# Kernel optimization log

Measured on AMD Instinct MI355X. Metric: run time of the kernel, lower is better.

Reference implementation:

```python
import jax, jax.numpy as jnp
import numpy as np

B, A, F = 8192, 8, 256      # batch, n_agents, per-agent obs feature dim
NA = 16                     # n_actions per agent
H1, H2 = 1024, 1024
OBS_D = A * F               # 2048 flattened obs dim
ACT_D = A * NA              # 128 joint action dim
IN_D = OBS_D + ACT_D        # 2176 MLP input dim


def setup_inputs() -> dict:
    key = jax.random.key(0)
    ks = jax.random.split(key, 8)
    s = 0.02
    return {
        "obs": jax.random.normal(ks[0], (B, A, F), dtype=jnp.float32),
        "all_actions": jax.random.uniform(ks[1], (B, ACT_D), dtype=jnp.float32),
        # per-agent stacked MLP params (agent axis first)
        "W1": jax.random.normal(ks[2], (A, IN_D, H1), dtype=jnp.float32) * s,
        "b1": jnp.zeros((A, H1), dtype=jnp.float32),
        "W2": jax.random.normal(ks[3], (A, H1, H2), dtype=jnp.float32) * s,
        "b2": jnp.zeros((A, H2), dtype=jnp.float32),
        "W3": jax.random.normal(ks[4], (A, H2, NA), dtype=jnp.float32) * s,
        "b3": jnp.zeros((A, NA), dtype=jnp.float32),
    }


def reference(obs, all_actions, W1, b1, W2, b2, W3, b3):
    b_s = obs.shape[0]
    obs_flat = obs.reshape(b_s, OBS_D)                      # [B, A*F]
    # mask[a, g] = 0 on agent a's own action block, 1 elsewhere
    mask = 1.0 - jnp.repeat(jnp.eye(A, dtype=obs.dtype), NA, axis=1)  # [A, A*NA]
    # split W1 into obs / action columns (equivalent to concat-then-dense)
    W1o = W1[:, :OBS_D, :]                                  # [A, OBS_D, H1]
    W1a = W1[:, OBS_D:, :]                                  # [A, ACT_D, H1]
    h1 = jax.nn.relu(
        jnp.einsum("bd,adh->bah", obs_flat, W1o)
        + jnp.einsum("bg,ag,agh->bah", all_actions, mask, W1a)
        + b1
    )                                                        # [B, A, H1]
    h2 = jax.nn.relu(jnp.einsum("bah,ahk->bak", h1, W2) + b2)  # [B, A, H2]
    out = jnp.einsum("bak,akn->ban", h2, W3) + b3              # [B, A, NA]
    return out.reshape(b_s, A * NA)
```

## Files before the change

kernel.cpp:

```cpp
#include <hip/hip_runtime.h>
#include <hip/hip_bf16.h>
#include <cstdint>
#include <cstddef>

typedef __bf16 bf16;
typedef __attribute__((ext_vector_type(8))) __bf16 bf16x8;
typedef __attribute__((ext_vector_type(4))) float f32x4;
typedef __attribute__((ext_vector_type(4))) int i32x4;
typedef __attribute__((address_space(3))) const bf16* lds_cp;

#define B_SZ  8192
#define NAGENT 8
#define NA_N  16
#define OBS_DD 2048
#define ACT_DD 128
#define IN_DD 2176
#define H1_D  1024
#define H2_D  1024

#define BM 256
#define BN 256
#define BK 64
#define GRID_M (B_SZ / BM)
#define GRID_N (1024 / BN)

__device__ __forceinline__ void gload16(const void* g, void* l) {
    __builtin_amdgcn_global_load_lds(
        (__attribute__((address_space(1))) void*)(g),
        (__attribute__((address_space(3))) void*)(l), 16, 0, 0);
}


__global__ void k_convert_x(const float* __restrict__ obs,
                            const float* __restrict__ act,
                            bf16* __restrict__ xb) {
    const int chunks = IN_DD / 8;
    int idx = blockIdx.x * blockDim.x + threadIdx.x;
    if (idx >= B_SZ * chunks) return;
    int b = idx / chunks;
    int c8 = idx - b * chunks;
    const float* src = (c8 < OBS_DD / 8)
        ? (obs + (size_t)b * OBS_DD + c8 * 8)
        : (act + (size_t)b * ACT_DD + (c8 - OBS_DD / 8) * 8);
    float4 v0 = ((const float4*)src)[0];
    float4 v1 = ((const float4*)src)[1];
    bf16x8 o;
    o[0] = (bf16)v0.x; o[1] = (bf16)v0.y; o[2] = (bf16)v0.z; o[3] = (bf16)v0.w;
    o[4] = (bf16)v1.x; o[5] = (bf16)v1.y; o[6] = (bf16)v1.z; o[7] = (bf16)v1.w;
    ((bf16x8*)(xb + (size_t)b * IN_DD))[c8] = o;
}

__global__ void k_transpose_w(const float* __restrict__ src, bf16* __restrict__ dst,
                              int K, int H, int maskStart) {
    __shared__ float tile[32][33];
    int a = blockIdx.z;
    int k0 = blockIdx.x * 32, h0 = blockIdx.y * 32;
    const float* s = src + (size_t)a * K * H;
    bf16* d = dst + (size_t)a * K * H;
    int tx = threadIdx.x, ty = threadIdx.y;
    #pragma unroll
    for (int i = 0; i < 32; i += 8) {
        int k = k0 + ty + i;
        float v = s[(size_t)k * H + h0 + tx];
        if (k >= maskStart) {
            int g = k - maskStart;
            if ((g >> 4) == a) v = 0.f;
        }
        tile[ty + i][tx] = v;
    }
    __syncthreads();
    #pragma unroll
    for (int i = 0; i < 32; i += 8) {
        d[(size_t)(h0 + ty + i) * K + k0 + tx] = (bf16)tile[tx][ty + i];
    }
}

__global__ void k_transpose_w3(const float* __restrict__ src, bf16* __restrict__ dst) {
    int idx = blockIdx.x * blockDim.x + threadIdx.x;
    if (idx >= NAGENT * NA_N * H2_D) return;
    int a = idx / (NA_N * H2_D);
    int n = (idx / H2_D) % NA_N;
    int k = idx % H2_D;
    dst[idx] = (bf16)src[(size_t)a * H2_D * NA_N + (size_t)k * NA_N + n];
}

__global__ void k_init_out(const float* __restrict__ b3, float* __restrict__ out) {
    int i = blockIdx.x * blockDim.x + threadIdx.x;
    if (i < B_SZ * NAGENT * NA_N) out[i] = b3[i & 127];
}

#define DSR4(d0, d1, d2, d3, addr, O0, O1, O2, O3)                      \
    asm volatile("ds_read_b128 %0, %4 offset:" #O0 "\n\t"               \
                 "ds_read_b128 %1, %4 offset:" #O1 "\n\t"               \
                 "ds_read_b128 %2, %4 offset:" #O2 "\n\t"               \
                 "ds_read_b128 %3, %4 offset:" #O3                      \
                 : "=&v"(d0), "=&v"(d1), "=&v"(d2), "=&v"(d3)           \
                 : "v"(addr))

#define BC(x) __builtin_bit_cast(bf16x8, x)

template<int FUSE>
__global__ __launch_bounds__(512, 2)
void k_gemm256(const bf16* __restrict__ Ain, size_t aStride, int lda,
               const bf16* __restrict__ Bw, const float* __restrict__ bias,
               bf16* __restrict__ Cout, size_t cStride, int K,
               int aOff, int gridZ,
               const bf16* __restrict__ W3Tp, float* __restrict__ outp) {
    extern __shared__ bf16 lds[];

    const int tid = threadIdx.x;
    const int w = tid >> 6;
    const int l = tid & 63;

    int flat = blockIdx.x + GRID_M * (blockIdx.y + GRID_N * blockIdx.z);
    int q8 = (GRID_M * GRID_N * gridZ) >> 3;
    int lin2 = (flat & 7) * q8 + (flat >> 3);
    const int mt = lin2 % GRID_M;
    int rest = lin2 / GRID_M;
    const int ntile = rest % GRID_N;
    const int az = rest / GRID_N;
    const int aw = az + aOff;

    const int rowBase = mt * BM;
    const int colBase = ntile * BN;
    const bf16* Aag = Ain + (size_t)az * aStride;
    const bf16* Bag = Bw + (size_t)aw * (size_t)1024 * K;

    const int wr = (w >> 2) * 128;
    const int wc = (w & 3) * 64;
    const int lr = l & 15;
    const int lq = l >> 4;

    const int rowA = (wr + lr) * BK;
    const int rowB = (wc + lr) * BK;
    const int ck0 = ((lq ^ (lr & 7)) * 8);
    const int ck1 = (((4 + lq) ^ (lr & 7)) * 8);

    const int sRow = w * 16 + (l >> 3);
    const int sCol = ((l & 7) ^ (l >> 3)) * 8;

    const bf16* pA0 = Aag + (size_t)(rowBase + sRow) * lda + sCol;
    const bf16* pA1 = Aag + (size_t)(rowBase + 128 + sRow) * lda + sCol;
    const bf16* pB0 = Bag + (size_t)(colBase + sRow) * K + sCol;
    const bf16* pB1 = Bag + (size_t)(colBase + 128 + sRow) * K + sCol;
    const size_t l8a = (size_t)8 * lda;
    const size_t l8b = (size_t)8 * K;

    const int nkt = K / BK;

#define STAGE_A(t1, half) do {                                              \
        const bf16* g_ = ((half) ? pA1 : pA0) + (t1) * BK;                  \
        bf16* d_ = &lds[(((t1) & 1) * 32768) + (half) * 8192 + w * 1024];   \
        gload16(g_, d_);                                                    \
        gload16(g_ + l8a, d_ + 512);                                        \
    } while (0)
#define STAGE_B(t2, half) do {                                              \
        const bf16* g_ = ((half) ? pB1 : pB0) + (t2) * BK;                  \
        bf16* d_ = &lds[(((t2) & 1) * 32768) + 16384 + (half) * 8192 + w * 1024]; \
        gload16(g_, d_);                                                    \
        gload16(g_ + l8b, d_ + 512);                                        \
    } while (0)

    f32x4 acc[8][4] = {};
    i32x4 ra0, ra1, ra2, ra3;
    i32x4 rb0, rb1, rb2, rb3;
    i32x4 rc0, rc1, rc2, rc3;

    STAGE_A(0, 0); STAGE_A(0, 1);
    STAGE_B(0, 0); STAGE_B(0, 1);
    if (nkt > 1) { STAGE_B(1, 0); STAGE_B(1, 1); }
    asm volatile("s_waitcnt vmcnt(0)" ::: "memory");
    __builtin_amdgcn_s_barrier();

    for (int t = 0; t < nkt; ++t) {
        const int dbuf = (t & 1) * 32768;
        lds_cp adrA0 = (lds_cp)lds + (dbuf + rowA + ck0);
        lds_cp adrA1 = (lds_cp)lds + (dbuf + rowA + ck1);
        lds_cp adrB0 = (lds_cp)lds + (dbuf + 16384 + rowB + ck0);
        lds_cp adrB1 = (lds_cp)lds + (dbuf + 16384 + rowB + ck1);

        DSR4(ra0, ra1, ra2, ra3, adrA0, 0, 2048, 4096, 6144);
        DSR4(rb0, rb1, rb2, rb3, adrB0, 0, 2048, 4096, 6144);
        if (t + 1 < nkt) STAGE_A(t + 1, 0);
        __builtin_amdgcn_s_barrier();
        asm volatile("s_waitcnt lgkmcnt(0)" ::: "memory");
        __builtin_amdgcn_sched_barrier(0);
        __builtin_amdgcn_s_setprio(1);
        #pragma unroll
        for (int n = 0; n < 4; ++n) {
            bf16x8 bv = BC(n == 0 ? rb0 : n == 1 ? rb1 : n == 2 ? rb2 : rb3);
            acc[0][n] = __builtin_amdgcn_mfma_f32_16x16x32_bf16(BC(ra0), bv, acc[0][n], 0, 0, 0);
            acc[1][n] = __builtin_amdgcn_mfma_f32_16x16x32_bf16(BC(ra1), bv, acc[1][n], 0, 0, 0);
            acc[2][n] = __builtin_amdgcn_mfma_f32_16x16x32_bf16(BC(ra2), bv, acc[2][n], 0, 0, 0);
            acc[3][n] = __builtin_amdgcn_mfma_f32_16x16x32_bf16(BC(ra3), bv, acc[3][n], 0, 0, 0);
        }
        __builtin_amdgcn_s_setprio(0);
        __builtin_amdgcn_s_barrier();

        DSR4(ra0, ra1, ra2, ra3, adrA0, 8192, 10240, 12288, 14336);
        DSR4(rc0, rc1, rc2, rc3, adrB1, 0, 2048, 4096, 6144);
        if (t + 1 < nkt) STAGE_A(t + 1, 1);
        __builtin_amdgcn_s_barrier();
        asm volatile("s_waitcnt lgkmcnt(0)" ::: "memory");
        __builtin_amdgcn_sched_barrier(0);
        __builtin_amdgcn_s_setprio(1);
        #pragma unroll
        for (int n = 0; n < 4; ++n) {
            bf16x8 bv = BC(n == 0 ? rb0 : n == 1 ? rb1 : n == 2 ? rb2 : rb3);
            acc[4][n] = __builtin_amdgcn_mfma_f32_16x16x32_bf16(BC(ra0), bv, acc[4][n], 0, 0, 0);
            acc[5][n] = __builtin_amdgcn_mfma_f32_16x16x32_bf16(BC(ra1), bv, acc[5][n], 0, 0, 0);
            acc[6][n] = __builtin_amdgcn_mfma_f32_16x16x32_bf16(BC(ra2), bv, acc[6][n], 0, 0, 0);
            acc[7][n] = __builtin_amdgcn_mfma_f32_16x16x32_bf16(BC(ra3), bv, acc[7][n], 0, 0, 0);
        }
        __builtin_amdgcn_s_setprio(0);
        __builtin_amdgcn_s_barrier();

        DSR4(ra0, ra1, ra2, ra3, adrA1, 0, 2048, 4096, 6144);
        if (t + 2 < nkt) STAGE_B(t + 2, 0);
        __builtin_amdgcn_s_barrier();
        asm volatile("s_waitcnt lgkmcnt(0)" ::: "memory");
        __builtin_amdgcn_sched_barrier(0);
        __builtin_amdgcn_s_setprio(1);
        #pragma unroll
        for (int n = 0; n < 4; ++n) {
            bf16x8 bv = BC(n == 0 ? rc0 : n == 1 ? rc1 : n == 2 ? rc2 : rc3);
            acc[0][n] = __builtin_amdgcn_mfma_f32_16x16x32_bf16(BC(ra0), bv, acc[0][n], 0, 0, 0);
            acc[1][n] = __builtin_amdgcn_mfma_f32_16x16x32_bf16(BC(ra1), bv, acc[1][n], 0, 0, 0);
            acc[2][n] = __builtin_amdgcn_mfma_f32_16x16x32_bf16(BC(ra2), bv, acc[2][n], 0, 0, 0);
            acc[3][n] = __builtin_amdgcn_mfma_f32_16x16x32_bf16(BC(ra3), bv, acc[3][n], 0, 0, 0);
        }
        __builtin_amdgcn_s_setprio(0);
        __builtin_amdgcn_s_barrier();

        DSR4(ra0, ra1, ra2, ra3, adrA1, 8192, 10240, 12288, 14336);
        if (t + 2 < nkt) STAGE_B(t + 2, 1);
        __builtin_amdgcn_s_barrier();
        asm volatile("s_waitcnt lgkmcnt(0)" ::: "memory");
        __builtin_amdgcn_sched_barrier(0);
        __builtin_amdgcn_s_setprio(1);
        #pragma unroll
        for (int n = 0; n < 4; ++n) {
            bf16x8 bv = BC(n == 0 ? rc0 : n == 1 ? rc1 : n == 2 ? rc2 : rc3);
            acc[4][n] = __builtin_amdgcn_mfma_f32_16x16x32_bf16(BC(ra0), bv, acc[4][n], 0, 0, 0);
            acc[5][n] = __builtin_amdgcn_mfma_f32_16x16x32_bf16(BC(ra1), bv, acc[5][n], 0, 0, 0);
            acc[6][n] = __builtin_amdgcn_mfma_f32_16x16x32_bf16(BC(ra2), bv, acc[6][n], 0, 0, 0);
            acc[7][n] = __builtin_amdgcn_mfma_f32_16x16x32_bf16(BC(ra3), bv, acc[7][n], 0, 0, 0);
        }
        __builtin_amdgcn_s_setprio(0);
        if (t < nkt - 2) {
            asm volatile("s_waitcnt vmcnt(4)" ::: "memory");
        } else {
            asm volatile("s_waitcnt vmcnt(0)" ::: "memory");
        }
        __builtin_amdgcn_s_barrier();
    }
#undef STAGE_A
#undef STAGE_B

    __syncthreads();
    const float* bAg = bias + (size_t)aw * 1024;
    float bb4[4];
    #pragma unroll
    for (int n = 0; n < 4; ++n) bb4[n] = bAg[colBase + wc + n * 16 + lr];
    #pragma unroll
    for (int m = 0; m < 8; ++m)
        #pragma unroll
        for (int n = 0; n < 4; ++n)
            #pragma unroll
            for (int r = 0; r < 4; ++r) {
                float v = acc[m][n][r] + bb4[n];
                v = fmaxf(v, 0.f);
                int row = wr + m * 16 + lq * 4 + r;
                int col = wc + n * 16 + lr;
                lds[row * 256 + ((((col >> 3) ^ (row & 7)) << 3) | (col & 7))] = (bf16)v;
            }
    __syncthreads();

    if constexpr (!FUSE) {
        bf16* Cg = Cout + (size_t)az * cStride + (size_t)rowBase * 1024 + colBase;
        const int er = tid >> 5;
        const int ec = tid & 31;
        #pragma unroll
        for (int i = 0; i < 16; ++i) {
            int row = i * 16 + er;
            int phys = ec ^ (row & 7);
            *(bf16x8*)&Cg[(size_t)row * 1024 + ec * 8] =
                *(const bf16x8*)&lds[row * 256 + phys * 8];
        }
    } else {
        const bf16* w3a = W3Tp + (size_t)aw * NA_N * H2_D;
        f32x4 oacc[2] = {};
        const int frow0 = w * 32;
        #pragma unroll
        for (int ks = 0; ks < 8; ++ks) {
            bf16x8 bfrag = *(const bf16x8*)&w3a[(size_t)lr * H2_D + colBase + ks * 32 + lq * 8];
            #pragma unroll
            for (int mm = 0; mm < 2; ++mm) {
                int row = frow0 + mm * 16 + lr;
                int lc = (ks * 4 + lq) ^ (row & 7);
                bf16x8 afrag = *(const bf16x8*)&lds[row * 256 + lc * 8];
                oacc[mm] = __builtin_amdgcn_mfma_f32_16x16x32_bf16(afrag, bfrag, oacc[mm], 0, 0, 0);
            }
        }
        #pragma unroll
        for (int mm = 0; mm < 2; ++mm)
            #pragma unroll
            for (int r = 0; r < 4; ++r)
                atomicAdd(&outp[(size_t)(rowBase + frow0 + mm * 16 + lq * 4 + r) * 128
                                + aw * NA_N + lr], oacc[mm][r]);
    }
}

extern "C" void kernel_launch(void* const* d_in, const int* in_sizes, int n_in,
                              void* d_out, int out_size, void* d_ws, size_t ws_size,
                              hipStream_t stream) {
    const float* obs = (const float*)d_in[0];
    const float* act = (const float*)d_in[1];
    const float* W1 = (const float*)d_in[2];
    const float* b1 = (const float*)d_in[3];
    const float* W2 = (const float*)d_in[4];
    const float* b2 = (const float*)d_in[5];
    const float* W3 = (const float*)d_in[6];
    const float* b3 = (const float*)d_in[7];
    float* out = (float*)d_out;

    const size_t SZ_XB  = (size_t)B_SZ * IN_DD * 2;
    const size_t SZ_W1T = (size_t)NAGENT * H1_D * IN_DD * 2;
    const size_t SZ_W2T = (size_t)NAGENT * H1_D * H2_D * 2;
    const size_t SZ_W3T = (size_t)NAGENT * NA_N * H2_D * 2;
    const size_t SZ_H1  = (size_t)B_SZ * H1_D * 2;
    const size_t SZ_FIX = SZ_XB + SZ_W1T + SZ_W2T + SZ_W3T;

    char* ws = (char*)d_ws;
    bf16* Xb  = (bf16*)ws;
    bf16* W1T = (bf16*)(ws + SZ_XB);
    bf16* W2T = (bf16*)(ws + SZ_XB + SZ_W1T);
    bf16* W3T = (bf16*)(ws + SZ_XB + SZ_W1T + SZ_W2T);
    char* hbase = ws + SZ_FIX;

    int G = 8;
    while (G > 1 && ws_size < SZ_FIX + (size_t)G * SZ_H1) G >>= 1;

    (void)hipFuncSetAttribute((const void*)k_gemm256<0>,
                              hipFuncAttributeMaxDynamicSharedMemorySize, 131072);
    (void)hipFuncSetAttribute((const void*)k_gemm256<1>,
                              hipFuncAttributeMaxDynamicSharedMemorySize, 131072);

    k_init_out<<<(B_SZ * 128 + 255) / 256, 256, 0, stream>>>(b3, out);

    {
        int n = B_SZ * (IN_DD / 8);
        k_convert_x<<<(n + 255) / 256, 256, 0, stream>>>(obs, act, Xb);
    }
    k_transpose_w<<<dim3(IN_DD / 32, H1_D / 32, NAGENT), dim3(32, 8), 0, stream>>>(
        W1, W1T, IN_DD, H1_D, OBS_DD);
    k_transpose_w<<<dim3(H1_D / 32, H2_D / 32, NAGENT), dim3(32, 8), 0, stream>>>(
        W2, W2T, H1_D, H2_D, 1 << 30);
    {
        int n = NAGENT * NA_N * H2_D;
        k_transpose_w3<<<(n + 255) / 256, 256, 0, stream>>>(W3, W3T);
    }

    const size_t agElems = (size_t)B_SZ * H1_D;
    bf16* h1 = (bf16*)hbase;

    for (int g0 = 0; g0 < NAGENT; g0 += G) {
        k_gemm256<0><<<dim3(GRID_M, GRID_N, G), 512, 131072, stream>>>(
            Xb, 0, IN_DD, W1T, b1, h1, agElems, IN_DD, g0, G, nullptr, nullptr);
        k_gemm256<1><<<dim3(GRID_M, GRID_N, G), 512, 131072, stream>>>(
            h1, agElems, H1_D, W2T, b2, nullptr, 0, H1_D, g0, G, W3T, out);
    }
    (void)in_sizes; (void)n_in; (void)out_size;
}
```

Baseline: 472.1 us.

## Switch GEMM mainloop to BK=32 with four-stage LDS ring pipeline

Halves the K-tile to 32 and replaces the two-buffer LDS scheme with a four-slot ring that prefetches three tiles ahead, staging A and B for tile t+3 while computing tile t. Hand-written ds_read_b128 inline asm and explicit lgkmcnt waits are replaced by plain vector LDS loads, leaving scheduling to the compiler. The intent is deeper latency hiding of global loads and fewer barriers per MFMA. In exchange each iteration does less MFMA work relative to its barriers, the swizzle narrows to 4 chunks, and the compiler may place LDS waits less carefully than the manual asm did.

```diff
diff --git a/kernel.cpp b/kernel.cpp
--- a/kernel.cpp
+++ b/kernel.cpp
@@ -6,8 +6,6 @@
 typedef __bf16 bf16;
 typedef __attribute__((ext_vector_type(8))) __bf16 bf16x8;
 typedef __attribute__((ext_vector_type(4))) float f32x4;
-typedef __attribute__((ext_vector_type(4))) int i32x4;
-typedef __attribute__((address_space(3))) const bf16* lds_cp;
 
 #define B_SZ  8192
 #define NAGENT 8
@@ -20,7 +18,7 @@
 
 #define BM 256
 #define BN 256
-#define BK 64
+#define BK 32
 #define GRID_M (B_SZ / BM)
 #define GRID_N (1024 / BN)
 
@@ -89,16 +87,6 @@
     if (i < B_SZ * NAGENT * NA_N) out[i] = b3[i & 127];
 }
 
-#define DSR4(d0, d1, d2, d3, addr, O0, O1, O2, O3)                      \
-    asm volatile("ds_read_b128 %0, %4 offset:" #O0 "\n\t"               \
-                 "ds_read_b128 %1, %4 offset:" #O1 "\n\t"               \
-                 "ds_read_b128 %2, %4 offset:" #O2 "\n\t"               \
-                 "ds_read_b128 %3, %4 offset:" #O3                      \
-                 : "=&v"(d0), "=&v"(d1), "=&v"(d2), "=&v"(d3)           \
-                 : "v"(addr))
-
-#define BC(x) __builtin_bit_cast(bf16x8, x)
-
 template<int FUSE>
 __global__ __launch_bounds__(512, 2)
 void k_gemm256(const bf16* __restrict__ Ain, size_t aStride, int lda,
@@ -131,123 +119,81 @@
     const int lr = l & 15;
     const int lq = l >> 4;
 
-    const int rowA = (wr + lr) * BK;
-    const int rowB = (wc + lr) * BK;
-    const int ck0 = ((lq ^ (lr & 7)) * 8);
-    const int ck1 = (((4 + lq) ^ (lr & 7)) * 8);
-
-    const int sRow = w * 16 + (l >> 3);
-    const int sCol = ((l & 7) ^ (l >> 3)) * 8;
-
-    const bf16* pA0 = Aag + (size_t)(rowBase + sRow) * lda + sCol;
-    const bf16* pA1 = Aag + (size_t)(rowBase + 128 + sRow) * lda + sCol;
-    const bf16* pB0 = Bag + (size_t)(colBase + sRow) * K + sCol;
-    const bf16* pB1 = Bag + (size_t)(colBase + 128 + sRow) * K + sCol;
-    const size_t l8a = (size_t)8 * lda;
-    const size_t l8b = (size_t)8 * K;
+    const int swz = (lq ^ (lr & 3)) * 8;
+    const int rA = (wr + lr) * 32 + swz;
+    const int rB = 8192 + (wc + lr) * 32 + swz;
+
+    const int sR = w * 16 + (l >> 2);
+    const int sC = ((l & 3) ^ ((l >> 2) & 3)) * 8;
+    const bf16* pA0 = Aag + (size_t)(rowBase + sR) * lda + sC;
+    const bf16* pA1 = Aag + (size_t)(rowBase + 128 + sR) * lda + sC;
+    const bf16* pB0 = Bag + (size_t)(colBase + sR) * K + sC;
+    const bf16* pB1 = Bag + (size_t)(colBase + 128 + sR) * K + sC;
 
     const int nkt = K / BK;
 
-#define STAGE_A(t1, half) do {                                              \
-        const bf16* g_ = ((half) ? pA1 : pA0) + (t1) * BK;                  \
-        bf16* d_ = &lds[(((t1) & 1) * 32768) + (half) * 8192 + w * 1024];   \
-        gload16(g_, d_);                                                    \
-        gload16(g_ + l8a, d_ + 512);                                        \
+#define STAGE_A(t3) do {                                                    \
+        bf16* d_ = &lds[(((t3) & 3) * 16384) + w * 512];                    \
+        gload16(pA0 + (t3) * BK, d_);                                       \
+        gload16(pA1 + (t3) * BK, d_ + 4096);                                \
     } while (0)
-#define STAGE_B(t2, half) do {                                              \
-        const bf16* g_ = ((half) ? pB1 : pB0) + (t2) * BK;                  \
-        bf16* d_ = &lds[(((t2) & 1) * 32768) + 16384 + (half) * 8192 + w * 1024]; \
-        gload16(g_, d_);                                                    \
-        gload16(g_ + l8b, d_ + 512);                                        \
+#define STAGE_B(t3) do {                                                    \
+        bf16* d_ = &lds[(((t3) & 3) * 16384) + 8192 + w * 512];             \
+        gload16(pB0 + (t3) * BK, d_);                                       \
+        gload16(pB1 + (t3) * BK, d_ + 4096);                                \
     } while (0)
 
     f32x4 acc[8][4] = {};
-    i32x4 ra0, ra1, ra2, ra3;
-    i32x4 rb0, rb1, rb2, rb3;
-    i32x4 rc0, rc1, rc2, rc3;
-
-    STAGE_A(0, 0); STAGE_A(0, 1);
-    STAGE_B(0, 0); STAGE_B(0, 1);
-    if (nkt > 1) { STAGE_B(1, 0); STAGE_B(1, 1); }
-    asm volatile("s_waitcnt vmcnt(0)" ::: "memory");
+    bf16x8 av0, av1, av2, av3, bv[4];
+
+    STAGE_A(0); STAGE_B(0);
+    STAGE_A(1); STAGE_B(1);
+    STAGE_A(2); STAGE_B(2);
+    asm volatile("s_waitcnt vmcnt(8)" ::: "memory");
     __builtin_amdgcn_s_barrier();
 
     for (int t = 0; t < nkt; ++t) {
-        const int dbuf = (t & 1) * 32768;
-        lds_cp adrA0 = (lds_cp)lds + (dbuf + rowA + ck0);
-        lds_cp adrA1 = (lds_cp)lds + (dbuf + rowA + ck1);
-        lds_cp adrB0 = (lds_cp)lds + (dbuf + 16384 + rowB + ck0);
-        lds_cp adrB1 = (lds_cp)lds + (dbuf + 16384 + rowB + ck1);
-
-        DSR4(ra0, ra1, ra2, ra3, adrA0, 0, 2048, 4096, 6144);
-        DSR4(rb0, rb1, rb2, rb3, adrB0, 0, 2048, 4096, 6144);
-        if (t + 1 < nkt) STAGE_A(t + 1, 0);
+        const int sb = (t & 3) * 16384;
+
+        av0 = *(const bf16x8*)&lds[sb + rA + 0 * 512];
+        av1 = *(const bf16x8*)&lds[sb + rA + 1 * 512];
+        av2 = *(const bf16x8*)&lds[sb + rA + 2 * 512];
+        av3 = *(const bf16x8*)&lds[sb + rA + 3 * 512];
+        bv[0] = *(const bf16x8*)&lds[sb + rB + 0 * 512];
+        bv[1] = *(const bf16x8*)&lds[sb + rB + 1 * 512];
+        bv[2] = *(const bf16x8*)&lds[sb + rB + 2 * 512];
+        bv[3] = *(const bf16x8*)&lds[sb + rB + 3 * 512];
+        if (t + 3 < nkt) STAGE_A(t + 3);
         __builtin_amdgcn_s_barrier();
-        asm volatile("s_waitcnt lgkmcnt(0)" ::: "memory");
-        __builtin_amdgcn_sched_barrier(0);
         __builtin_amdgcn_s_setprio(1);
         #pragma unroll
         for (int n = 0; n < 4; ++n) {
-            bf16x8 bv = BC(n == 0 ? rb0 : n == 1 ? rb1 : n == 2 ? rb2 : rb3);
-            acc[0][n] = __builtin_amdgcn_mfma_f32_16x16x32_bf16(BC(ra0), bv, acc[0][n], 0, 0, 0);
-            acc[1][n] = __builtin_amdgcn_mfma_f32_16x16x32_bf16(BC(ra1), bv, acc[1][n], 0, 0, 0);
-            acc[2][n] = __builtin_amdgcn_mfma_f32_16x16x32_bf16(BC(ra2), bv, acc[2][n], 0, 0, 0);
-            acc[3][n] = __builtin_amdgcn_mfma_f32_16x16x32_bf16(BC(ra3), bv, acc[3][n], 0, 0, 0);
+            acc[0][n] = __builtin_amdgcn_mfma_f32_16x16x32_bf16(av0, bv[n], acc[0][n], 0, 0, 0);
+            acc[1][n] = __builtin_amdgcn_mfma_f32_16x16x32_bf16(av1, bv[n], acc[1][n], 0, 0, 0);
+            acc[2][n] = __builtin_amdgcn_mfma_f32_16x16x32_bf16(av2, bv[n], acc[2][n], 0, 0, 0);
+            acc[3][n] = __builtin_amdgcn_mfma_f32_16x16x32_bf16(av3, bv[n], acc[3][n], 0, 0, 0);
         }
         __builtin_amdgcn_s_setprio(0);
         __builtin_amdgcn_s_barrier();
 
-        DSR4(ra0, ra1, ra2, ra3, adrA0, 8192, 10240, 12288, 14336);
-        DSR4(rc0, rc1, rc2, rc3, adrB1, 0, 2048, 4096, 6144);
-        if (t + 1 < nkt) STAGE_A(t + 1, 1);
+        av0 = *(const bf16x8*)&lds[sb + rA + 4 * 512];
+        av1 = *(const bf16x8*)&lds[sb + rA + 5 * 512];
+        av2 = *(const bf16x8*)&lds[sb + rA + 6 * 512];
+        av3 = *(const bf16x8*)&lds[sb + rA + 7 * 512];
+        if (t + 3 < nkt) STAGE_B(t + 3);
         __builtin_amdgcn_s_barrier();
-        asm volatile("s_waitcnt lgkmcnt(0)" ::: "memory");
-        __builtin_amdgcn_sched_barrier(0);
         __builtin_amdgcn_s_setprio(1);
         #pragma unroll
         for (int n = 0; n < 4; ++n) {
-            bf16x8 bv = BC(n == 0 ? rb0 : n == 1 ? rb1 : n == 2 ? rb2 : rb3);
-            acc[4][n] = __builtin_amdgcn_mfma_f32_16x16x32_bf16(BC(ra0), bv, acc[4][n], 0, 0, 0);
-            acc[5][n] = __builtin_amdgcn_mfma_f32_16x16x32_bf16(BC(ra1), bv, acc[5][n], 0, 0, 0);
-            acc[6][n] = __builtin_amdgcn_mfma_f32_16x16x32_bf16(BC(ra2), bv, acc[6][n], 0, 0, 0);
-            acc[7][n] = __builtin_amdgcn_mfma_f32_16x16x32_bf16(BC(ra3), bv, acc[7][n], 0, 0, 0);
+            acc[4][n] = __builtin_amdgcn_mfma_f32_16x16x32_bf16(av0, bv[n], acc[4][n], 0, 0, 0);
+            acc[5][n] = __builtin_amdgcn_mfma_f32_16x16x32_bf16(av1, bv[n], acc[5][n], 0, 0, 0);
+            acc[6][n] = __builtin_amdgcn_mfma_f32_16x16x32_bf16(av2, bv[n], acc[6][n], 0, 0, 0);
+            acc[7][n] = __builtin_amdgcn_mfma_f32_16x16x32_bf16(av3, bv[n], acc[7][n], 0, 0, 0);
         }
         __builtin_amdgcn_s_setprio(0);
-        __builtin_amdgcn_s_barrier();
-
-        DSR4(ra0, ra1, ra2, ra3, adrA1, 0, 2048, 4096, 6144);
-        if (t + 2 < nkt) STAGE_B(t + 2, 0);
-        __builtin_amdgcn_s_barrier();
-        asm volatile("s_waitcnt lgkmcnt(0)" ::: "memory");
-        __builtin_amdgcn_sched_barrier(0);
-        __builtin_amdgcn_s_setprio(1);
-        #pragma unroll
-        for (int n = 0; n < 4; ++n) {
-            bf16x8 bv = BC(n == 0 ? rc0 : n == 1 ? rc1 : n == 2 ? rc2 : rc3);
-            acc[0][n] = __builtin_amdgcn_mfma_f32_16x16x32_bf16(BC(ra0), bv, acc[0][n], 0, 0, 0);
-            acc[1][n] = __builtin_amdgcn_mfma_f32_16x16x32_bf16(BC(ra1), bv, acc[1][n], 0, 0, 0);
-            acc[2][n] = __builtin_amdgcn_mfma_f32_16x16x32_bf16(BC(ra2), bv, acc[2][n], 0, 0, 0);
-            acc[3][n] = __builtin_amdgcn_mfma_f32_16x16x32_bf16(BC(ra3), bv, acc[3][n], 0, 0, 0);
-        }
-        __builtin_amdgcn_s_setprio(0);
-        __builtin_amdgcn_s_barrier();
-
-        DSR4(ra0, ra1, ra2, ra3, adrA1, 8192, 10240, 12288, 14336);
-        if (t + 2 < nkt) STAGE_B(t + 2, 1);
-        __builtin_amdgcn_s_barrier();
-        asm volatile("s_waitcnt lgkmcnt(0)" ::: "memory");
-        __builtin_amdgcn_sched_barrier(0);
-        __builtin_amdgcn_s_setprio(1);
-        #pragma unroll
-        for (int n = 0; n < 4; ++n) {
-            bf16x8 bv = BC(n == 0 ? rc0 : n == 1 ? rc1 : n == 2 ? rc2 : rc3);
-            acc[4][n] = __builtin_amdgcn_mfma_f32_16x16x32_bf16(BC(ra0), bv, acc[4][n], 0, 0, 0);
-            acc[5][n] = __builtin_amdgcn_mfma_f32_16x16x32_bf16(BC(ra1), bv, acc[5][n], 0, 0, 0);
-            acc[6][n] = __builtin_amdgcn_mfma_f32_16x16x32_bf16(BC(ra2), bv, acc[6][n], 0, 0, 0);
-            acc[7][n] = __builtin_amdgcn_mfma_f32_16x16x32_bf16(BC(ra3), bv, acc[7][n], 0, 0, 0);
-        }
-        __builtin_amdgcn_s_setprio(0);
-        if (t < nkt - 2) {
+        if (t + 3 < nkt) {
+            asm volatile("s_waitcnt vmcnt(8)" ::: "memory");
+        } else if (t + 2 < nkt) {
             asm volatile("s_waitcnt vmcnt(4)" ::: "memory");
         } else {
             asm volatile("s_waitcnt vmcnt(0)" ::: "memory");
```

After: 509.2 us. +7.9%, slower.

## Restructure GEMM main loop: issue full next-tile prefetch upfront, drop intra-iteration barriers

Applied to the files above, without the earlier changes.

The main loop of the 256x256 GEMM is rebuilt so that all global-to-LDS loads for the next K tile are issued at the start of each iteration into a simple A/B double buffer. LDS fragments for the whole tile are read into extra register sets and consumed with staggered lgkmcnt waits, leaving only one barrier per iteration instead of several. Launch bounds drop to one block per CU, which frees registers for the larger fragment set but halves the occupancy available to hide latency. The previous deeper B prefetch (two tiles ahead) is removed, and a full vmcnt(0) wait now closes every iteration.

```diff
diff --git a/kernel.cpp b/kernel.cpp
--- a/kernel.cpp
+++ b/kernel.cpp
@@ -100,7 +100,7 @@
 #define BC(x) __builtin_bit_cast(bf16x8, x)
 
 template<int FUSE>
-__global__ __launch_bounds__(512, 2)
+__global__ __launch_bounds__(512, 1)
 void k_gemm256(const bf16* __restrict__ Ain, size_t aStride, int lda,
                const bf16* __restrict__ Bw, const float* __restrict__ bias,
                bf16* __restrict__ Cout, size_t cStride, int K,
@@ -138,7 +138,6 @@
 
     const int sRow = w * 16 + (l >> 3);
     const int sCol = ((l & 7) ^ (l >> 3)) * 8;
-
     const bf16* pA0 = Aag + (size_t)(rowBase + sRow) * lda + sCol;
     const bf16* pA1 = Aag + (size_t)(rowBase + 128 + sRow) * lda + sCol;
     const bf16* pB0 = Bag + (size_t)(colBase + sRow) * K + sCol;
@@ -150,13 +149,13 @@
 
 #define STAGE_A(t1, half) do {                                              \
         const bf16* g_ = ((half) ? pA1 : pA0) + (t1) * BK;                  \
-        bf16* d_ = &lds[(((t1) & 1) * 32768) + (half) * 8192 + w * 1024];   \
+        bf16* d_ = &lds[(((t1) & 1) * 16384) + (half) * 8192 + w * 1024];   \
         gload16(g_, d_);                                                    \
         gload16(g_ + l8a, d_ + 512);                                        \
     } while (0)
 #define STAGE_B(t2, half) do {                                              \
         const bf16* g_ = ((half) ? pB1 : pB0) + (t2) * BK;                  \
-        bf16* d_ = &lds[(((t2) & 1) * 32768) + 16384 + (half) * 8192 + w * 1024]; \
+        bf16* d_ = &lds[32768 + (((t2) & 1) * 16384) + (half) * 8192 + w * 1024]; \
         gload16(g_, d_);                                                    \
         gload16(g_ + l8b, d_ + 512);                                        \
     } while (0)
@@ -165,97 +164,84 @@
     i32x4 ra0, ra1, ra2, ra3;
     i32x4 rb0, rb1, rb2, rb3;
     i32x4 rc0, rc1, rc2, rc3;
+    i32x4 rd0, rd1, rd2, rd3;
+    i32x4 re0, re1, re2, re3;
+    i32x4 rf0, rf1, rf2, rf3;
+
+#define MFMA16(ACC0, A0, A1, A2, A3, B0, B1, B2, B3)                        \
+    do {                                                                    \
+        acc[ACC0+0][0] = __builtin_amdgcn_mfma_f32_16x16x32_bf16(BC(A0), BC(B0), acc[ACC0+0][0], 0, 0, 0); \
+        acc[ACC0+1][0] = __builtin_amdgcn_mfma_f32_16x16x32_bf16(BC(A1), BC(B0), acc[ACC0+1][0], 0, 0, 0); \
+        acc[ACC0+2][0] = __builtin_amdgcn_mfma_f32_16x16x32_bf16(BC(A2), BC(B0), acc[ACC0+2][0], 0, 0, 0); \
+        acc[ACC0+3][0] = __builtin_amdgcn_mfma_f32_16x16x32_bf16(BC(A3), BC(B0), acc[ACC0+3][0], 0, 0, 0); \
+        acc[ACC0+0][1] = __builtin_amdgcn_mfma_f32_16x16x32_bf16(BC(A0), BC(B1), acc[ACC0+0][1], 0, 0, 0); \
+        acc[ACC0+1][1] = __builtin_amdgcn_mfma_f32_16x16x32_bf16(BC(A1), BC(B1), acc[ACC0+1][1], 0, 0, 0); \
+        acc[ACC0+2][1] = __builtin_amdgcn_mfma_f32_16x16x32_bf16(BC(A2), BC(B1), acc[ACC0+2][1], 0, 0, 0); \
+        acc[ACC0+3][1] = __builtin_amdgcn_mfma_f32_16x16x32_bf16(BC(A3), BC(B1), acc[ACC0+3][1], 0, 0, 0); \
+        acc[ACC0+0][2] = __builtin_amdgcn_mfma_f32_16x16x32_bf16(BC(A0), BC(B2), acc[ACC0+0][2], 0, 0, 0); \
+        acc[ACC0+1][2] = __builtin_amdgcn_mfma_f32_16x16x32_bf16(BC(A1), BC(B2), acc[ACC0+1][2], 0, 0, 0); \
+        acc[ACC0+2][2] = __builtin_amdgcn_mfma_f32_16x16x32_bf16(BC(A2), BC(B2), acc[ACC0+2][2], 0, 0, 0); \
+        acc[ACC0+3][2] = __builtin_amdgcn_mfma_f32_16x16x32_bf16(BC(A3), BC(B2), acc[ACC0+3][2], 0, 0, 0); \
+        acc[ACC0+0][3] = __builtin_amdgcn_mfma_f32_16x16x32_bf16(BC(A0), BC(B3), acc[ACC0+0][3], 0, 0, 0); \
+        acc[ACC0+1][3] = __builtin_amdgcn_mfma_f32_16x16x32_bf16(BC(A1), BC(B3), acc[ACC0+1][3], 0, 0, 0); \
+        acc[ACC0+2][3] = __builtin_amdgcn_mfma_f32_16x16x32_bf16(BC(A2), BC(B3), acc[ACC0+2][3], 0, 0, 0); \
+        acc[ACC0+3][3] = __builtin_amdgcn_mfma_f32_16x16x32_bf16(BC(A3), BC(B3), acc[ACC0+3][3], 0, 0, 0); \
+    } while (0)
 
     STAGE_A(0, 0); STAGE_A(0, 1);
     STAGE_B(0, 0); STAGE_B(0, 1);
-    if (nkt > 1) { STAGE_B(1, 0); STAGE_B(1, 1); }
     asm volatile("s_waitcnt vmcnt(0)" ::: "memory");
     __builtin_amdgcn_s_barrier();
 
     for (int t = 0; t < nkt; ++t) {
-        const int dbuf = (t & 1) * 32768;
+        const int dbuf = (t & 1) * 16384;
         lds_cp adrA0 = (lds_cp)lds + (dbuf + rowA + ck0);
         lds_cp adrA1 = (lds_cp)lds + (dbuf + rowA + ck1);
-        lds_cp adrB0 = (lds_cp)lds + (dbuf + 16384 + rowB + ck0);
-        lds_cp adrB1 = (lds_cp)lds + (dbuf + 16384 + rowB + ck1);
+        lds_cp adrB0 = (lds_cp)lds + (32768 + dbuf + rowB + ck0);
+        lds_cp adrB1 = (lds_cp)lds + (32768 + dbuf + rowB + ck1);
+
+        if (t + 1 < nkt) {
+            STAGE_A(t + 1, 0); STAGE_A(t + 1, 1);
+            STAGE_B(t + 1, 0); STAGE_B(t + 1, 1);
+        }
 
         DSR4(ra0, ra1, ra2, ra3, adrA0, 0, 2048, 4096, 6144);
         DSR4(rb0, rb1, rb2, rb3, adrB0, 0, 2048, 4096, 6144);
-        if (t + 1 < nkt) STAGE_A(t + 1, 0);
-        __builtin_amdgcn_s_barrier();
+        DSR4(rc0, rc1, rc2, rc3, adrA0, 8192, 10240, 12288, 14336);
+        DSR4(rd0, rd1, rd2, rd3, adrB1, 0, 2048, 4096, 6144);
+
+        asm volatile("s_waitcnt lgkmcnt(8)" ::: "memory");
+        __builtin_amdgcn_sched_barrier(0);
+        __builtin_amdgcn_s_setprio(1);
+        MFMA16(0, ra0, ra1, ra2, ra3, rb0, rb1, rb2, rb3);
+        __builtin_amdgcn_s_setprio(0);
+
+        DSR4(re0, re1, re2, re3, adrA1, 0, 2048, 4096, 6144);
+        asm volatile("s_waitcnt lgkmcnt(4)" ::: "memory");
+        __builtin_amdgcn_sched_barrier(0);
+        __builtin_amdgcn_s_setprio(1);
+        MFMA16(4, rc0, rc1, rc2, rc3, rb0, rb1, rb2, rb3);
+        __builtin_amdgcn_s_setprio(0);
+
+        DSR4(rf0, rf1, rf2, rf3, adrA1, 8192, 10240, 12288, 14336);
+        asm volatile("s_waitcnt lgkmcnt(4)" ::: "memory");
+        __builtin_amdgcn_sched_barrier(0);
+        __builtin_amdgcn_s_setprio(1);
+        MFMA16(0, re0, re1, re2, re3, rd0, rd1, rd2, rd3);
+        __builtin_amdgcn_s_setprio(0);
+
         asm volatile("s_waitcnt lgkmcnt(0)" ::: "memory");
         __builtin_amdgcn_sched_barrier(0);
         __builtin_amdgcn_s_setprio(1);
-        #pragma unroll
-        for (int n = 0; n < 4; ++n) {
-            bf16x8 bv = BC(n == 0 ? rb0 : n == 1 ? rb1 : n == 2 ? rb2 : rb3);
-            acc[0][n] = __builtin_amdgcn_mfma_f32_16x16x32_bf16(BC(ra0), bv, acc[0][n], 0, 0, 0);
-            acc[1][n] = __builtin_amdgcn_mfma_f32_16x16x32_bf16(BC(ra1), bv, acc[1][n], 0, 0, 0);
-            acc[2][n] = __builtin_amdgcn_mfma_f32_16x16x32_bf16(BC(ra2), bv, acc[2][n], 0, 0, 0);
-            acc[3][n] = __builtin_amdgcn_mfma_f32_16x16x32_bf16(BC(ra3), bv, acc[3][n], 0, 0, 0);
-        }
+        MFMA16(4, rf0, rf1, rf2, rf3, rd0, rd1, rd2, rd3);
         __builtin_amdgcn_s_setprio(0);
-        __builtin_amdgcn_s_barrier();
-
-        DSR4(ra0, ra1, ra2, ra3, adrA0, 8192, 10240, 12288, 14336);
-        DSR4(rc0, rc1, rc2, rc3, adrB1, 0, 2048, 4096, 6144);
-        if (t + 1 < nkt) STAGE_A(t + 1, 1);
-        __builtin_amdgcn_s_barrier();
-        asm volatile("s_waitcnt lgkmcnt(0)" ::: "memory");
-        __builtin_amdgcn_sched_barrier(0);
-        __builtin_amdgcn_s_setprio(1);
-        #pragma unroll
-        for (int n = 0; n < 4; ++n) {
-            bf16x8 bv = BC(n == 0 ? rb0 : n == 1 ? rb1 : n == 2 ? rb2 : rb3);
-            acc[4][n] = __builtin_amdgcn_mfma_f32_16x16x32_bf16(BC(ra0), bv, acc[4][n], 0, 0, 0);
-            acc[5][n] = __builtin_amdgcn_mfma_f32_16x16x32_bf16(BC(ra1), bv, acc[5][n], 0, 0, 0);
-            acc[6][n] = __builtin_amdgcn_mfma_f32_16x16x32_bf16(BC(ra2), bv, acc[6][n], 0, 0, 0);
-            acc[7][n] = __builtin_amdgcn_mfma_f32_16x16x32_bf16(BC(ra3), bv, acc[7][n], 0, 0, 0);
-        }
-        __builtin_amdgcn_s_setprio(0);
-        __builtin_amdgcn_s_barrier();
-
-        DSR4(ra0, ra1, ra2, ra3, adrA1, 0, 2048, 4096, 6144);
-        if (t + 2 < nkt) STAGE_B(t + 2, 0);
-        __builtin_amdgcn_s_barrier();
-        asm volatile("s_waitcnt lgkmcnt(0)" ::: "memory");
-        __builtin_amdgcn_sched_barrier(0);
-        __builtin_amdgcn_s_setprio(1);
-        #pragma unroll
-        for (int n = 0; n < 4; ++n) {
-            bf16x8 bv = BC(n == 0 ? rc0 : n == 1 ? rc1 : n == 2 ? rc2 : rc3);
-            acc[0][n] = __builtin_amdgcn_mfma_f32_16x16x32_bf16(BC(ra0), bv, acc[0][n], 0, 0, 0);
-            acc[1][n] = __builtin_amdgcn_mfma_f32_16x16x32_bf16(BC(ra1), bv, acc[1][n], 0, 0, 0);
-            acc[2][n] = __builtin_amdgcn_mfma_f32_16x16x32_bf16(BC(ra2), bv, acc[2][n], 0, 0, 0);
-            acc[3][n] = __builtin_amdgcn_mfma_f32_16x16x32_bf16(BC(ra3), bv, acc[3][n], 0, 0, 0);
-        }
-        __builtin_amdgcn_s_setprio(0);
-        __builtin_amdgcn_s_barrier();
-
-        DSR4(ra0, ra1, ra2, ra3, adrA1, 8192, 10240, 12288, 14336);
-        if (t + 2 < nkt) STAGE_B(t + 2, 1);
-        __builtin_amdgcn_s_barrier();
-        asm volatile("s_waitcnt lgkmcnt(0)" ::: "memory");
-        __builtin_amdgcn_sched_barrier(0);
-        __builtin_amdgcn_s_setprio(1);
-        #pragma unroll
-        for (int n = 0; n < 4; ++n) {
-            bf16x8 bv = BC(n == 0 ? rc0 : n == 1 ? rc1 : n == 2 ? rc2 : rc3);
-            acc[4][n] = __builtin_amdgcn_mfma_f32_16x16x32_bf16(BC(ra0), bv, acc[4][n], 0, 0, 0);
-            acc[5][n] = __builtin_amdgcn_mfma_f32_16x16x32_bf16(BC(ra1), bv, acc[5][n], 0, 0, 0);
-            acc[6][n] = __builtin_amdgcn_mfma_f32_16x16x32_bf16(BC(ra2), bv, acc[6][n], 0, 0, 0);
-            acc[7][n] = __builtin_amdgcn_mfma_f32_16x16x32_bf16(BC(ra3), bv, acc[7][n], 0, 0, 0);
-        }
-        __builtin_amdgcn_s_setprio(0);
-        if (t < nkt - 2) {
-            asm volatile("s_waitcnt vmcnt(4)" ::: "memory");
-        } else {
-            asm volatile("s_waitcnt vmcnt(0)" ::: "memory");
-        }
+
+        asm volatile("s_waitcnt vmcnt(0)" ::: "memory");
         __builtin_amdgcn_s_barrier();
     }
 #undef STAGE_A
 #undef STAGE_B
+#undef MFMA16
 
     __syncthreads();
     const float* bAg = bias + (size_t)aw * 1024;
```

New measurement: 454.2 us. 3.8% less time.
